# Optimization experiments

Hardware: AMD Instinct MI355X
Metric: run time of the kernel (lower is better)

## Reference

```python
import jax, jax.numpy as jnp
import numpy as np

DIM = -1
ALPHA = 1.5
N_ITERS = 100


def _p(z):
    # p(z) = clamp(z, min=0) ** (1 / (alpha - 1)); for alpha=1.5 this is square
    return jnp.maximum(z, 0.0) ** (1.0 / (ALPHA - 1.0))


def entmax_bisect(X):
    """Bisection search for the entmax threshold tau (entmax_bisect, alpha=1.5)."""
    am1 = ALPHA - 1.0
    d = X.shape[DIM]
    Xs = X * am1                                   # scaled logits
    max_val = jnp.max(Xs, axis=DIM, keepdims=True)
    tau_lo = max_val - 1.0                         # gp(1) = 1**(alpha-1) = 1
    tau_hi = max_val - (1.0 / d) ** am1            # gp(1/d)
    f_lo = jnp.sum(_p(Xs - tau_lo), axis=DIM, keepdims=True) - 1.0
    dm0 = tau_hi - tau_lo

    def body(i, carry):
        tau_lo, dm, _ = carry
        dm = dm * 0.5
        tau_m = tau_lo + dm
        p_m = _p(Xs - tau_m)
        f_m = jnp.sum(p_m, axis=DIM, keepdims=True) - 1.0
        tau_lo = jnp.where(f_m * f_lo >= 0.0, tau_m, tau_lo)
        return (tau_lo, dm, p_m)

    p0 = jnp.zeros_like(Xs)
    _, _, p_m = jax.lax.fori_loop(0, N_ITERS, body, (tau_lo, dm0, p0))
    # ensure_sum_one normalization (as in the entmax library forward)
    return p_m / jnp.sum(p_m, axis=DIM, keepdims=True)


def setup_inputs() -> dict:
    key = jax.random.key(0)
    x = jax.random.normal(key, (2, 1024, 32000), dtype=jnp.float32)
    return {"x": x}


def reference(x):
    # LogEntmaxBisect.forward: log(entmax_bisect(x, dim, alpha, iters))
    # zero-probability entries yield -inf, matching torch.log(0.)
    return jnp.log(entmax_bisect(x))
```

## Files before the change

kernel.cpp:

```cpp
#include <hip/hip_runtime.h>
#include <float.h>
#include <math.h>

#define D_DIM   32000
#define NT      256
#define CHUNKS  (D_DIM / 4)
#define KITER   ((CHUNKS + NT - 1) / NT)
#define NG4     (KITER / 4)
#define NWAVES  (NT / 64)
#define CAPW    1200

typedef float f32x4 __attribute__((ext_vector_type(4)));
typedef unsigned long long ull;

__device__ __forceinline__ float waveReduceSum(float v) {
#pragma unroll
    for (int m = 32; m >= 1; m >>= 1) v += __shfl_xor(v, m, 64);
    return v;
}

__device__ __forceinline__ float waveReduceMax(float v) {
#pragma unroll
    for (int m = 32; m >= 1; m >>= 1) v = fmaxf(v, __shfl_xor(v, m, 64));
    return v;
}

__device__ __forceinline__ float scrub_finite(float v) {
    const unsigned u = __float_as_uint(v);
    if ((u & 0x7f800000u) == 0x7f800000u) return -FLT_MAX;
    return v;
}

__device__ __forceinline__ float4 ldg4(const float4* __restrict__ p, int c) {
    if (c < CHUNKS) return p[c];
    float4 r; r.x = r.y = r.z = r.w = -FLT_MAX;
    return r;
}

__global__ __launch_bounds__(NT, 8)
void entmax_log_fused(const float* __restrict__ x, float* __restrict__ out, int rows)
{
    const int row = blockIdx.x;
    if (row >= rows) return;
    const size_t base = (size_t)row * D_DIM;
    const float4* __restrict__ xr4 = reinterpret_cast<const float4*>(x + base);
    float* __restrict__ orow = out + base;

    __shared__ __align__(16) float s_pool[NWAVES * CAPW];
    __shared__ float s_red[NWAVES];
    __shared__ int   s_cnt[NWAVES];
    __shared__ int   s_flag;
    __shared__ float2 s_ts;

    const int lane = threadIdx.x & 63;
    const int wv   = threadIdx.x >> 6;
    float* __restrict__ wpool = s_pool + wv * CAPW;
    const ull lmask = (1ull << lane) - 1ull;

    if (threadIdx.x == 0) s_flag = 0;
    __syncthreads();

    float runL  = -FLT_MAX;
    float waveM = -FLT_MAX;
    float pendR = -FLT_MAX;
    int n = 0;
    bool ovf = false;

    float4 cur[4], nxt[4];
#pragma unroll
    for (int j = 0; j < 4; ++j) cur[j] = ldg4(xr4, threadIdx.x + j * NT);

    for (int g = 0; g < NG4; ++g) {
        if (g + 1 < NG4) {
#pragma unroll
            for (int j = 0; j < 4; ++j)
                nxt[j] = ldg4(xr4, threadIdx.x + ((g + 1) * 4 + j) * NT);
        }
        float z[16];
#pragma unroll
        for (int j = 0; j < 4; ++j) {
            z[4 * j + 0] = cur[j].x; z[4 * j + 1] = cur[j].y;
            z[4 * j + 2] = cur[j].z; z[4 * j + 3] = cur[j].w;
        }
        float cm = z[0];
#pragma unroll
        for (int i = 1; i < 16; ++i) cm = fmaxf(cm, z[i]);
        runL = fmaxf(runL, cm);
        if ((g & 1) == 0) {
            waveM = fmaxf(waveM, pendR);
            pendR = waveReduceMax(runL);
        }

        float thrL = fmaxf(runL, waveM) - 2.0f;
        ull msk[16];
        int tot = 0;
#pragma unroll
        for (int j = 0; j < 16; ++j) {
            msk[j] = __ballot(z[j] > thrL);
            tot += __popcll(msk[j]);
        }
        if (tot) {
            if (n + tot > CAPW) {
                const float wfresh = waveReduceMax(runL);
                waveM = fmaxf(waveM, wfresh);
                const float thrW = wfresh - 2.0f;
                int nn = 0;
                for (int i = 0; i < n; i += 64) {
                    const float v = (i + lane < n) ? wpool[i + lane] : -FLT_MAX;
                    const ull km = __ballot(v > thrW);
                    const int r = __popcll(km & lmask);
                    if (v > thrW) wpool[nn + r] = v;
                    nn += __popcll(km);
                }
                n = nn;
                thrL = fmaxf(runL, waveM) - 2.0f;
                tot = 0;
#pragma unroll
                for (int j = 0; j < 16; ++j) {
                    msk[j] = __ballot(z[j] > thrL);
                    tot += __popcll(msk[j]);
                }
            }
            if (n + tot > CAPW) {
                ovf = true;
            } else {
#pragma unroll
                for (int j = 0; j < 16; ++j) {
                    if (z[j] > thrL) {
                        const int r = __popcll(msk[j] & lmask);
                        wpool[n + r] = z[j];
                    }
                    n += __popcll(msk[j]);
                }
            }
        }
#pragma unroll
        for (int j = 0; j < 4; ++j) cur[j] = nxt[j];
    }
    if (ovf && lane == 0) s_flag = 1;

    if (lane == 0) s_red[wv] = waveReduceMax(runL);
    __syncthreads();
    const float max_val = fmaxf(fmaxf(s_red[0], s_red[1]), fmaxf(s_red[2], s_red[3]));
    const int flag = s_flag;
    __syncthreads();

    const float u_lo0 = max_val - 2.0f;
    const float u_hi  = max_val - 0.011180339887498949f;

    if (!flag) {
        {
            int nn = 0;
            for (int i = 0; i < n; i += 64) {
                const float v = (i + lane < n) ? wpool[i + lane] : -FLT_MAX;
                const ull km = __ballot(v > u_lo0);
                const int r = __popcll(km & lmask);
                if (v > u_lo0) wpool[nn + r] = v;
                nn += __popcll(km);
            }
            if (lane == 0) s_cnt[wv] = nn;
        }
        __syncthreads();

        if (wv == 0) {
            const int n0 = s_cnt[0], n1 = s_cnt[1], n2 = s_cnt[2], n3 = s_cnt[3];

#define POOL_SCAN2(uv, acc2, acc1)                                             \
            do {                                                               \
                const float* __restrict__ pp0 = s_pool;                        \
                for (int i = lane; i < n0; i += 64) {                          \
                    const float t = fmaxf(pp0[i] - (uv), 0.0f);                \
                    acc2 = fmaf(t, t, acc2); acc1 += t;                        \
                }                                                              \
                const float* __restrict__ pp1 = s_pool + CAPW;                 \
                for (int i = lane; i < n1; i += 64) {                          \
                    const float t = fmaxf(pp1[i] - (uv), 0.0f);                \
                    acc2 = fmaf(t, t, acc2); acc1 += t;                        \
                }                                                              \
                const float* __restrict__ pp2 = s_pool + 2 * CAPW;             \
                for (int i = lane; i < n2; i += 64) {                          \
                    const float t = fmaxf(pp2[i] - (uv), 0.0f);                \
                    acc2 = fmaf(t, t, acc2); acc1 += t;                        \
                }                                                              \
                const float* __restrict__ pp3 = s_pool + 3 * CAPW;             \
                for (int i = lane; i < n3; i += 64) {                          \
                    const float t = fmaxf(pp3[i] - (uv), 0.0f);                \
                    acc2 = fmaf(t, t, acc2); acc1 += t;                        \
                }                                                              \
            } while (0)

            float u = u_lo0;
            float s_v = 4.0f;
            for (int it = 0; it < 24; ++it) {
                float S2 = 0.0f, S1 = 0.0f;
                POOL_SCAN2(u, S2, S1);
                S2 = waveReduceSum(S2);
                S1 = waveReduceSum(S1);
                s_v = S2;
                const float g = S2 - 4.0f;
                if (g <= 0.0f) break;
                const float u_new = fminf(u + g / (2.0f * S1), u_hi);
                if (u_new == u) break;
                u = u_new;
            }
#undef POOL_SCAN2
            if (lane == 0) { s_ts.x = u; s_ts.y = s_v; }
        }
        __syncthreads();
    } else {
        float u_lo = u_lo0;
        float acc = 0.0f;
        for (int k = 0; k < KITER; ++k) {
            const int c = threadIdx.x + k * NT;
            if (c < CHUNKS) {
                const float4 v = xr4[c];
                float t;
                t = fmaxf(v.x - u_lo, 0.0f); acc = fmaf(t, t, acc);
                t = fmaxf(v.y - u_lo, 0.0f); acc = fmaf(t, t, acc);
                t = fmaxf(v.z - u_lo, 0.0f); acc = fmaf(t, t, acc);
                t = fmaxf(v.w - u_lo, 0.0f); acc = fmaf(t, t, acc);
            }
        }
        acc = waveReduceSum(acc);
        if (lane == 0) s_red[wv] = acc;
        __syncthreads();
        const float f_lo = (s_red[0] + s_red[1] + s_red[2] + s_red[3]) - 4.0f;
        __syncthreads();

        float dm = u_hi - u_lo;
        float u_m = u_lo;
        float s_v = 4.0f;
        for (int it = 0; it < 100; ++it) {
            dm *= 0.5f;
            u_m = u_lo + dm;
            const bool fixed = (u_m == u_lo);
            float a = 0.0f;
            for (int k = 0; k < KITER; ++k) {
                const int c = threadIdx.x + k * NT;
                if (c < CHUNKS) {
                    const float4 v = xr4[c];
                    float t;
                    t = fmaxf(v.x - u_m, 0.0f); a = fmaf(t, t, a);
                    t = fmaxf(v.y - u_m, 0.0f); a = fmaf(t, t, a);
                    t = fmaxf(v.z - u_m, 0.0f); a = fmaf(t, t, a);
                    t = fmaxf(v.w - u_m, 0.0f); a = fmaf(t, t, a);
                }
            }
            a = waveReduceSum(a);
            if (lane == 0) s_red[wv] = a;
            __syncthreads();
            const float s = s_red[0] + s_red[1] + s_red[2] + s_red[3];
            __syncthreads();
            s_v = s;
            if ((s - 4.0f) * f_lo >= 0.0f) u_lo = u_m;
            if (fixed) break;
        }
        if (threadIdx.x == 0) { s_ts.x = u_m; s_ts.y = s_v; }
        __syncthreads();
    }

    const float u_m = s_ts.x;
    const float inv_sv = 1.0f / s_ts.y;
    const f32x4* __restrict__ xv4 = reinterpret_cast<const f32x4*>(x + base);
    for (int k = 0; k < KITER; ++k) {
        const int c = threadIdx.x + k * NT;
        if (c < CHUNKS) {
            const f32x4 v = __builtin_nontemporal_load(xv4 + c);
            f32x4 o;
            {
                const float t = fmaxf(v.x - u_m, 0.0f);
                o.x = scrub_finite(__logf(fmaxf(t * t, 1e-35f) * inv_sv));
            }
            {
                const float t = fmaxf(v.y - u_m, 0.0f);
                o.y = scrub_finite(__logf(fmaxf(t * t, 1e-35f) * inv_sv));
            }
            {
                const float t = fmaxf(v.z - u_m, 0.0f);
                o.z = scrub_finite(__logf(fmaxf(t * t, 1e-35f) * inv_sv));
            }
            {
                const float t = fmaxf(v.w - u_m, 0.0f);
                o.w = scrub_finite(__logf(fmaxf(t * t, 1e-35f) * inv_sv));
            }
            __builtin_nontemporal_store(o, reinterpret_cast<f32x4*>(orow) + c);
        }
    }
}

extern "C" void kernel_launch(void* const* d_in, const int* in_sizes, int n_in,
                              void* d_out, int out_size, void* d_ws, size_t ws_size,
                              hipStream_t stream) {
    const float* x = (const float*)d_in[0];
    float* out = (float*)d_out;
    const int rows = in_sizes[0] / D_DIM;
    entmax_log_fused<<<dim3(rows), dim3(NT), 0, stream>>>(x, out, rows);
}
```

Measured before the change: 127.6 us.

## Split fused entmax into tau-search and finish kernels, fusing first Newton sum

```diff
diff --git a/kernel.cpp b/kernel.cpp
--- a/kernel.cpp
+++ b/kernel.cpp
@@ -38,19 +38,19 @@
 }
 
 __global__ __launch_bounds__(NT, 8)
-void entmax_log_fused(const float* __restrict__ x, float* __restrict__ out, int rows)
+void entmax_tau_kernel(const float* __restrict__ x, float* __restrict__ out, int rows)
 {
     const int row = blockIdx.x;
     if (row >= rows) return;
     const size_t base = (size_t)row * D_DIM;
     const float4* __restrict__ xr4 = reinterpret_cast<const float4*>(x + base);
-    float* __restrict__ orow = out + base;
 
     __shared__ __align__(16) float s_pool[NWAVES * CAPW];
     __shared__ float s_red[NWAVES];
+    __shared__ float s_S2[NWAVES];
+    __shared__ float s_S1[NWAVES];
     __shared__ int   s_cnt[NWAVES];
     __shared__ int   s_flag;
-    __shared__ float2 s_ts;
 
     const int lane = threadIdx.x & 63;
     const int wv   = threadIdx.x >> 6;
@@ -151,62 +151,65 @@
     if (!flag) {
         {
             int nn = 0;
+            float a2 = 0.0f, a1 = 0.0f;
             for (int i = 0; i < n; i += 64) {
                 const float v = (i + lane < n) ? wpool[i + lane] : -FLT_MAX;
                 const ull km = __ballot(v > u_lo0);
                 const int r = __popcll(km & lmask);
                 if (v > u_lo0) wpool[nn + r] = v;
                 nn += __popcll(km);
-            }
-            if (lane == 0) s_cnt[wv] = nn;
+                const float t = fmaxf(v - u_lo0, 0.0f);
+                a2 = fmaf(t, t, a2); a1 += t;
+            }
+            a2 = waveReduceSum(a2);
+            a1 = waveReduceSum(a1);
+            if (lane == 0) { s_cnt[wv] = nn; s_S2[wv] = a2; s_S1[wv] = a1; }
         }
         __syncthreads();
-
-        if (wv == 0) {
-            const int n0 = s_cnt[0], n1 = s_cnt[1], n2 = s_cnt[2], n3 = s_cnt[3];
-
-#define POOL_SCAN2(uv, acc2, acc1)                                             \
-            do {                                                               \
-                const float* __restrict__ pp0 = s_pool;                        \
-                for (int i = lane; i < n0; i += 64) {                          \
-                    const float t = fmaxf(pp0[i] - (uv), 0.0f);                \
-                    acc2 = fmaf(t, t, acc2); acc1 += t;                        \
-                }                                                              \
-                const float* __restrict__ pp1 = s_pool + CAPW;                 \
-                for (int i = lane; i < n1; i += 64) {                          \
-                    const float t = fmaxf(pp1[i] - (uv), 0.0f);                \
-                    acc2 = fmaf(t, t, acc2); acc1 += t;                        \
-                }                                                              \
-                const float* __restrict__ pp2 = s_pool + 2 * CAPW;             \
-                for (int i = lane; i < n2; i += 64) {                          \
-                    const float t = fmaxf(pp2[i] - (uv), 0.0f);                \
-                    acc2 = fmaf(t, t, acc2); acc1 += t;                        \
-                }                                                              \
-                const float* __restrict__ pp3 = s_pool + 3 * CAPW;             \
-                for (int i = lane; i < n3; i += 64) {                          \
-                    const float t = fmaxf(pp3[i] - (uv), 0.0f);                \
-                    acc2 = fmaf(t, t, acc2); acc1 += t;                        \
-                }                                                              \
-            } while (0)
-
-            float u = u_lo0;
-            float s_v = 4.0f;
-            for (int it = 0; it < 24; ++it) {
-                float S2 = 0.0f, S1 = 0.0f;
-                POOL_SCAN2(u, S2, S1);
-                S2 = waveReduceSum(S2);
-                S1 = waveReduceSum(S1);
-                s_v = S2;
-                const float g = S2 - 4.0f;
-                if (g <= 0.0f) break;
-                const float u_new = fminf(u + g / (2.0f * S1), u_hi);
-                if (u_new == u) break;
-                u = u_new;
-            }
-#undef POOL_SCAN2
-            if (lane == 0) { s_ts.x = u; s_ts.y = s_v; }
-        }
-        __syncthreads();
+        if (wv != 0) return;
+
+        const int n0 = s_cnt[0], n1 = s_cnt[1], n2 = s_cnt[2], n3 = s_cnt[3];
+        float u  = u_lo0;
+        float s_v = s_S2[0] + s_S2[1] + s_S2[2] + s_S2[3];
+        float g  = s_v - 4.0f;
+        float S1 = s_S1[0] + s_S1[1] + s_S1[2] + s_S1[3];
+
+        for (int it = 0; it < 24 && g > 0.0f; ++it) {
+            const float u_new = fminf(u + g / (2.0f * S1), u_hi);
+            if (u_new == u) break;
+            u = u_new;
+            float S2 = 0.0f; S1 = 0.0f;
+            {
+                const float* __restrict__ pp0 = s_pool;
+                for (int i = lane; i < n0; i += 64) {
+                    const float t = fmaxf(pp0[i] - u, 0.0f);
+                    S2 = fmaf(t, t, S2); S1 += t;
+                }
+                const float* __restrict__ pp1 = s_pool + CAPW;
+                for (int i = lane; i < n1; i += 64) {
+                    const float t = fmaxf(pp1[i] - u, 0.0f);
+                    S2 = fmaf(t, t, S2); S1 += t;
+                }
+                const float* __restrict__ pp2 = s_pool + 2 * CAPW;
+                for (int i = lane; i < n2; i += 64) {
+                    const float t = fmaxf(pp2[i] - u, 0.0f);
+                    S2 = fmaf(t, t, S2); S1 += t;
+                }
+                const float* __restrict__ pp3 = s_pool + 3 * CAPW;
+                for (int i = lane; i < n3; i += 64) {
+                    const float t = fmaxf(pp3[i] - u, 0.0f);
+                    S2 = fmaf(t, t, S2); S1 += t;
+                }
+            }
+            S2 = waveReduceSum(S2);
+            S1 = waveReduceSum(S1);
+            s_v = S2;
+            g = S2 - 4.0f;
+        }
+        if (lane == 0) {
+            float2 ts; ts.x = u; ts.y = s_v;
+            *reinterpret_cast<float2*>(out + base) = ts;
+        }
     } else {
         float u_lo = u_lo0;
         float acc = 0.0f;
@@ -255,13 +258,28 @@
             if ((s - 4.0f) * f_lo >= 0.0f) u_lo = u_m;
             if (fixed) break;
         }
-        if (threadIdx.x == 0) { s_ts.x = u_m; s_ts.y = s_v; }
-        __syncthreads();
+        if (threadIdx.x == 0) {
+            float2 ts; ts.x = u_m; ts.y = s_v;
+            *reinterpret_cast<float2*>(out + base) = ts;
+        }
     }
-
+}
+
+__global__ __launch_bounds__(NT, 8)
+void entmax_finish_kernel(const float* __restrict__ x, float* __restrict__ out, int rows)
+{
+    const int row = blockIdx.x;
+    if (row >= rows) return;
+    const size_t base = (size_t)row * D_DIM;
+    const f32x4* __restrict__ xv4 = reinterpret_cast<const f32x4*>(x + base);
+    float* __restrict__ orow = out + base;
+
+    __shared__ float2 s_ts;
+    if (threadIdx.x == 0) s_ts = *reinterpret_cast<const float2*>(orow);
+    __syncthreads();
     const float u_m = s_ts.x;
     const float inv_sv = 1.0f / s_ts.y;
-    const f32x4* __restrict__ xv4 = reinterpret_cast<const f32x4*>(x + base);
+
     for (int k = 0; k < KITER; ++k) {
         const int c = threadIdx.x + k * NT;
         if (c < CHUNKS) {
@@ -294,5 +312,6 @@
     const float* x = (const float*)d_in[0];
     float* out = (float*)d_out;
     const int rows = in_sizes[0] / D_DIM;
-    entmax_log_fused<<<dim3(rows), dim3(NT), 0, stream>>>(x, out, rows);
-}
+    entmax_tau_kernel<<<dim3(rows), dim3(NT), 0, stream>>>(x, out, rows);
+    entmax_finish_kernel<<<dim3(rows), dim3(NT), 0, stream>>>(x, out, rows);
+}
```

New measurement: 159.1 us. +24.7%, slower.
